# Kernel optimization log

Hardware: AMD Instinct MI355X
Metric: run time of the kernel (lower is better)

The kernel has to match this reference:

```python
import jax, jax.numpy as jnp
import numpy as np

B, S, D, H, HD = 2, 2048, 1024, 16, 64
DFF = 4 * D
EPS = 1e-6


def _rms(x, w):
    return w * (x * jax.lax.rsqrt(jnp.mean(x * x, axis=-1, keepdims=True) + EPS))


def _rope(x, rope):
    # x: [B, H, S, HD], rope: [S, HD, 2]
    cos = rope[..., 0][None, None]
    sin = rope[..., 1][None, None]
    xr = x.reshape(*x.shape[:-1], -1, 2)
    rot = jnp.stack([-xr[..., 1], xr[..., 0]], axis=-1).reshape(x.shape)
    return x * cos + rot * sin


def setup_inputs() -> dict:
    key = jax.random.key(0)
    ks = jax.random.split(key, 10)
    w = lambda k, shape: jax.random.normal(k, shape, jnp.float32) * 0.02
    return {
        "hidden_states": jax.random.normal(ks[0], (B, S, D), jnp.float32),
        "timestep": jax.random.normal(ks[1], (B, D), jnp.float32),
        "rope_pos_embed": jax.random.normal(ks[2], (S, HD, 2), jnp.float32),
        "adaln_w": w(ks[3], (6 * D, D)),
        "adaln_b": jnp.zeros((6 * D,), jnp.float32),
        "wq": w(ks[4], (D, D)),
        "wk": w(ks[5], (D, D)),
        "wv": w(ks[6], (D, D)),
        "wo": w(ks[7], (D, D)),
        "q_norm_w": jnp.ones((D,), jnp.float32),
        "k_norm_w": jnp.ones((D,), jnp.float32),
        "norm3_w": jnp.ones((D,), jnp.float32),
        "fc1_w": w(ks[8], (DFF, D)),
        "fc1_b": jnp.zeros((DFF,), jnp.float32),
        "fc2_w": w(ks[9], (D, DFF)),
        "fc2_b": jnp.zeros((D,), jnp.float32),
    }


def reference(hidden_states, timestep, rope_pos_embed, adaln_w, adaln_b,
              wq, wk, wv, wo, q_norm_w, k_norm_w, norm3_w,
              fc1_w, fc1_b, fc2_w, fc2_b):
    x = hidden_states  # [B, S, D]
    # AdaLayerNorm: emb = Linear(SiLU(timestep)) -> 6 modulation chunks, broadcast over seq
    emb = jax.nn.silu(timestep) @ adaln_w.T + adaln_b  # [B, 6D]
    sh_msa, sc_msa, g_msa, sh_mlp, sc_mlp, g_mlp = jnp.split(emb[:, None, :], 6, axis=-1)
    mu = jnp.mean(x, axis=-1, keepdims=True)
    var = jnp.mean((x - mu) ** 2, axis=-1, keepdims=True)
    ln = (x - mu) * jax.lax.rsqrt(var + EPS)
    xm = ln * (1.0 + sc_msa) + sh_msa  # modulated input to attention

    # Attention: projections + RMSNorm over inner_dim + RoPE + SDPA
    q = _rms(xm @ wq.T, q_norm_w)
    k = _rms(xm @ wk.T, k_norm_w)
    v = xm @ wv.T
    q = q.reshape(B, S, H, HD).transpose(0, 2, 1, 3)
    k = k.reshape(B, S, H, HD).transpose(0, 2, 1, 3)
    v = v.reshape(B, S, H, HD).transpose(0, 2, 1, 3)
    q = _rope(q, rope_pos_embed)
    k = _rope(k, rope_pos_embed)
    scores = jnp.einsum('bhqd,bhkd->bhqk', q, k) * (HD ** -0.5)
    attn = jax.nn.softmax(scores, axis=-1)
    o = jnp.einsum('bhqk,bhkd->bhqd', attn, v)
    o = o.transpose(0, 2, 1, 3).reshape(B, S, H * HD) @ wo.T

    h = x + g_msa * o  # gated residual

    # MLP branch with AdaLN scale/shift on RMSNorm output
    n3 = _rms(h, norm3_w)
    nm = n3 * (1.0 + sc_mlp) + sh_mlp
    ff = jax.nn.gelu(nm @ fc1_w.T + fc1_b, approximate=True) @ fc2_w.T + fc2_b
    return h + g_mlp * ff
```

## Files before the change

### kernel.cpp

```cpp
#include <hip/hip_runtime.h>
#include <cstdint>
#include <cstddef>

typedef unsigned short ushort_t;
typedef __attribute__((ext_vector_type(8))) short s8v;
typedef __attribute__((ext_vector_type(4))) short s4v;
typedef __attribute__((ext_vector_type(4))) float f4v;

#define MFMA16(a, b, c) __builtin_amdgcn_mfma_f32_16x16x32_bf16(a, b, c, 0, 0, 0)

__device__ __forceinline__ ushort_t f2bf(float f) {
  union { float f; unsigned u; } a; a.f = f;
  return (ushort_t)((a.u + 0x7fffu + ((a.u >> 16) & 1u)) >> 16);
}
__device__ __forceinline__ float bf2f(ushort_t h) {
  union { unsigned u; float f; } a; a.u = ((unsigned)h) << 16; return a.f;
}
__device__ __forceinline__ unsigned fbits(float f) {
  union { float f; unsigned u; } a; a.f = f; return a.u;
}

__device__ __forceinline__ void gload16(const void* g, void* l) {
  __builtin_amdgcn_global_load_lds(
      (__attribute__((address_space(1))) void*)(uintptr_t)g,
      (__attribute__((address_space(3))) void*)(unsigned)(uintptr_t)l,
      16, 0, 0);
}

__launch_bounds__(256)
__global__ void convert_w(const float* __restrict__ wq, const float* __restrict__ wk,
                          const float* __restrict__ wv, const float* __restrict__ wo,
                          const float* __restrict__ f1, const float* __restrict__ f2,
                          ushort_t* __restrict__ dqkv, ushort_t* __restrict__ dwo,
                          ushort_t* __restrict__ df1, ushort_t* __restrict__ df2)
{
  const int blk = blockIdx.x;
  const float* src; ushort_t* dst; int off;
  if      (blk < 1024) { src = wq; dst = dqkv;            off = blk; }
  else if (blk < 2048) { src = wk; dst = dqkv + 1048576;  off = blk - 1024; }
  else if (blk < 3072) { src = wv; dst = dqkv + 2097152;  off = blk - 2048; }
  else if (blk < 4096) { src = wo; dst = dwo;             off = blk - 3072; }
  else if (blk < 8192) { src = f1; dst = df1;             off = blk - 4096; }
  else                 { src = f2; dst = df2;             off = blk - 8192; }
  const int idx = off * 1024 + threadIdx.x * 4;
  float4 v = *(const float4*)(src + idx);
  s4v o;
  o[0] = (short)f2bf(v.x); o[1] = (short)f2bf(v.y);
  o[2] = (short)f2bf(v.z); o[3] = (short)f2bf(v.w);
  *(s4v*)(dst + idx) = o;
}

__launch_bounds__(256)
__global__ void adaln(const float* __restrict__ ts, const float* __restrict__ w,
                      const float* __restrict__ bias, float* __restrict__ emb)
{
  const int j = blockIdx.x * 4 + (threadIdx.x >> 6);
  const int lane = threadIdx.x & 63;
  const float* wr = w + (size_t)j * 1024;
  float s0 = 0.f, s1 = 0.f;
  for (int i = lane; i < 1024; i += 64) {
    const float wv = wr[i];
    const float t0 = ts[i], t1 = ts[1024 + i];
    const float e0 = __builtin_amdgcn_exp2f(-1.4426950409f * t0);
    const float e1 = __builtin_amdgcn_exp2f(-1.4426950409f * t1);
    s0 += wv * t0 * __builtin_amdgcn_rcpf(1.f + e0);
    s1 += wv * t1 * __builtin_amdgcn_rcpf(1.f + e1);
  }
  #pragma unroll
  for (int m = 32; m; m >>= 1) { s0 += __shfl_down(s0, m); s1 += __shfl_down(s1, m); }
  if (!lane) { emb[j] = s0 + bias[j]; emb[6144 + j] = s1 + bias[j]; }
}

__launch_bounds__(256)
__global__ void ln_mod(const float* __restrict__ x, const float* __restrict__ emb,
                       ushort_t* __restrict__ xm)
{
  const int row = blockIdx.x, b = row >> 11, tid = threadIdx.x;
  const float* xr = x + (size_t)row * 1024;
  const int c = tid * 4;
  float4 v = *(const float4*)(xr + c);
  float s  = v.x + v.y + v.z + v.w;
  float s2 = v.x*v.x + v.y*v.y + v.z*v.z + v.w*v.w;
  #pragma unroll
  for (int m = 32; m; m >>= 1) { s += __shfl_down(s, m); s2 += __shfl_down(s2, m); }
  __shared__ float red[8];
  const int wave = tid >> 6, lane = tid & 63;
  if (!lane) { red[wave] = s; red[4 + wave] = s2; }
  __syncthreads();
  const float mu = (red[0] + red[1] + red[2] + red[3]) * (1.f / 1024.f);
  const float ms = (red[4] + red[5] + red[6] + red[7]) * (1.f / 1024.f);
  const float rstd = rsqrtf(ms - mu * mu + 1e-6f);
  const float* sh = emb + b * 6144;
  const float* sc = emb + b * 6144 + 1024;
  float4 shv = *(const float4*)(sh + c);
  float4 scv = *(const float4*)(sc + c);
  s4v ov;
  ov[0] = (short)f2bf((v.x - mu) * rstd * (1.f + scv.x) + shv.x);
  ov[1] = (short)f2bf((v.y - mu) * rstd * (1.f + scv.y) + shv.y);
  ov[2] = (short)f2bf((v.z - mu) * rstd * (1.f + scv.z) + shv.z);
  ov[3] = (short)f2bf((v.w - mu) * rstd * (1.f + scv.w) + shv.w);
  *(s4v*)(xm + (size_t)row * 1024 + c) = ov;
}

template<int EPI, int TN>
__launch_bounds__(256, 4)
__global__ void gemm_bt(const ushort_t* __restrict__ A, const ushort_t* __restrict__ Bw,
                        int K, int N,
                        ushort_t* __restrict__ outb, float* __restrict__ outf,
                        const float* __restrict__ bias, const float* __restrict__ resid,
                        const float* __restrict__ emb, int gate_off)
{
  constexpr int JN = TN / 32;
  constexpr int BUFB = TN * 32;
  __shared__ ushort_t As0[128 * 32], As1[128 * 32];
  __shared__ ushort_t Bs0[BUFB],    Bs1[BUFB];
  const int tid = threadIdx.x;
  const int wave = tid >> 6, lane = tid & 63;
  const int quad = lane >> 4, r = lane & 15;
  const int m0 = blockIdx.y * 128, n0 = blockIdx.x * TN;
  const int wm = (wave >> 1) * 64, wn = (wave & 1) * (TN / 2);

  const int srow = wave * 16 + (lane >> 2);
  const int scol = (lane & 3) * 8;
  const ushort_t* ag = A  + (size_t)(m0 + srow) * K + scol;
  const ushort_t* bg = Bw + (size_t)(n0 + srow) * K + scol;
  const size_t rowK64 = (size_t)64 * K;

  f4v acc[4][JN] = {};

  auto stage = [&](ushort_t* as, ushort_t* bs) {
    gload16(ag,          as + wave * 512);
    gload16(ag + rowK64, as + wave * 512 + 2048);
    gload16(bg,          bs + wave * 512);
    if (TN == 128) gload16(bg + rowK64, bs + wave * 512 + 2048);
    ag += 32; bg += 32;
  };
  auto compute = [&](const ushort_t* ab, const ushort_t* bb) {
    s8v af[4], bf[JN];
    #pragma unroll
    for (int i = 0; i < 4; i++)
      af[i] = *(const s8v*)(ab + (wm + i * 16 + r) * 32 + quad * 8);
    #pragma unroll
    for (int j = 0; j < JN; j++)
      bf[j] = *(const s8v*)(bb + (wn + j * 16 + r) * 32 + quad * 8);
    #pragma unroll
    for (int i = 0; i < 4; i++)
      #pragma unroll
      for (int j = 0; j < JN; j++)
        acc[i][j] = MFMA16(af[i], bf[j], acc[i][j]);
  };

  stage(As0, Bs0);
  __syncthreads();
  const int R = (K >> 6) - 1;
  for (int it = 0; it < R; it++) {
    stage(As1, Bs1);
    compute(As0, Bs0);
    __syncthreads();
    stage(As0, Bs0);
    compute(As1, Bs1);
    __syncthreads();
  }
  stage(As1, Bs1);
  compute(As0, Bs0);
  __syncthreads();
  compute(As1, Bs1);

  const int bblk = m0 >> 11;
  float bj[JN], gj[JN];
  #pragma unroll
  for (int j = 0; j < JN; j++) {
    const int col = n0 + wn + j * 16 + r;
    bj[j] = (EPI == 2 || EPI == 3) ? bias[col] : 0.f;
    gj[j] = (EPI == 1 || EPI == 3) ? emb[bblk * 6144 + gate_off + col] : 0.f;
  }
  #pragma unroll
  for (int i = 0; i < 4; i++) {
    #pragma unroll
    for (int rr = 0; rr < 4; rr++) {
      const int row = m0 + wm + i * 16 + quad * 4 + rr;
      const size_t rbase = (size_t)row * N + n0 + wn;
      #pragma unroll
      for (int j = 0; j < JN; j++) {
        float v = acc[i][j][rr];
        const size_t idx = rbase + j * 16 + r;
        if (EPI == 0) {
          outb[idx] = f2bf(v);
        } else if (EPI == 1) {
          outf[idx] = resid[idx] + gj[j] * v;
        } else if (EPI == 2) {
          v += bj[j];
          const float t = fmaf(v * v, 0.1029436f, 2.3022083f);
          const float e = __builtin_amdgcn_exp2f(-v * t);
          outb[idx] = f2bf(v * __builtin_amdgcn_rcpf(1.f + e));
        } else {
          outf[idx] = resid[idx] + gj[j] * (v + bj[j]);
        }
      }
    }
  }
}

#define G8_PHASE(AB, BB, KS, MH, LOADB)                                       \
  {                                                                           \
    s8v af[4];                                                                \
    const int ck = ((((KS) << 2) | quad) ^ rx) << 3;                          \
    const ushort_t* Ap = (AB) + (wm + (MH) * 64 + r) * 64 + ck;               \
    af[0] = *(const s8v*)(Ap);                                                \
    af[1] = *(const s8v*)(Ap + 1024);                                         \
    af[2] = *(const s8v*)(Ap + 2048);                                         \
    af[3] = *(const s8v*)(Ap + 3072);                                         \
    if (LOADB) {                                                              \
      const ushort_t* Bp = (BB) + (wn + r) * 64 + ck;                         \
      bf[0] = *(const s8v*)(Bp);                                              \
      bf[1] = *(const s8v*)(Bp + 1024);                                       \
      bf[2] = *(const s8v*)(Bp + 2048);                                       \
      bf[3] = *(const s8v*)(Bp + 3072);                                       \
    }                                                                         \
    __builtin_amdgcn_s_barrier();                                             \
    __builtin_amdgcn_s_setprio(1);                                            \
    _Pragma("unroll")                                                         \
    for (int i_ = 0; i_ < 4; i_++) {                                          \
      _Pragma("unroll")                                                       \
      for (int j_ = 0; j_ < 4; j_++)                                          \
        acc[(MH) * 4 + i_][j_] = MFMA16(af[i_], bf[j_], acc[(MH) * 4 + i_][j_]); \
    }                                                                         \
    __builtin_amdgcn_s_setprio(0);                                            \
    __builtin_amdgcn_s_barrier();                                             \
  }

template<int EPI>
__launch_bounds__(512, 2)
__global__ void gemm8p(const ushort_t* __restrict__ A, const ushort_t* __restrict__ Bw,
                       int K, int N, ushort_t* __restrict__ outb,
                       const float* __restrict__ bias)
{
  __shared__ ushort_t Ash[2][256 * 64];
  __shared__ ushort_t Bsh[2][256 * 64];
  const int tid = threadIdx.x;
  const int wid = tid >> 6, lane = tid & 63;
  const int quad = lane >> 4, r = lane & 15, rx = r & 7;

  const int nwg = gridDim.x * gridDim.y;
  int wg = blockIdx.y * gridDim.x + blockIdx.x;
  wg = (wg & 7) * (nwg >> 3) + (wg >> 3);
  const int bx = wg % gridDim.x, by = wg / gridDim.x;
  const int m0 = by * 256, n0 = bx * 256;
  const int wm = (wid >> 2) * 128;
  const int wn = (wid & 3) * 64;

  const int srow = lane >> 3;
  const int scol = ((lane & 7) ^ srow) * 8;
  const ushort_t* ag = A  + (size_t)(m0 + wid * 32 + srow) * K + scol;
  const ushort_t* bg = Bw + (size_t)(n0 + wid * 32 + srow) * K + scol;
  const size_t row8K = (size_t)8 * K;

  f4v acc[8][4] = {};

  auto STAGE = [&](int buf, int kt) {
    const size_t ko = (size_t)kt * 64;
    ushort_t* Ad = &Ash[buf][wid * 2048];
    ushort_t* Bd = &Bsh[buf][wid * 2048];
    #pragma unroll
    for (int c = 0; c < 4; c++)
      gload16(ag + ko + c * row8K, Ad + c * 512);
    #pragma unroll
    for (int c = 0; c < 4; c++)
      gload16(bg + ko + c * row8K, Bd + c * 512);
  };

  STAGE(0, 0);
  STAGE(1, 1);
  asm volatile("s_waitcnt vmcnt(8)" ::: "memory");
  __builtin_amdgcn_s_barrier();

  const int NT = K >> 6;
  #pragma unroll 1
  for (int t = 0; t < NT; t += 2) {
    {
      const ushort_t* Ab = &Ash[0][0];
      const ushort_t* Bb = &Bsh[0][0];
      s8v bf[4];
      G8_PHASE(Ab, Bb, 0, 0, true);
      G8_PHASE(Ab, Bb, 0, 1, false);
      G8_PHASE(Ab, Bb, 1, 0, true);
      G8_PHASE(Ab, Bb, 1, 1, false);
      if (t + 2 < NT) {
        STAGE(0, t + 2);
        asm volatile("s_waitcnt vmcnt(8)" ::: "memory");
      } else {
        asm volatile("s_waitcnt vmcnt(0)" ::: "memory");
      }
      __builtin_amdgcn_s_barrier();
    }
    {
      const ushort_t* Ab = &Ash[1][0];
      const ushort_t* Bb = &Bsh[1][0];
      s8v bf[4];
      G8_PHASE(Ab, Bb, 0, 0, true);
      G8_PHASE(Ab, Bb, 0, 1, false);
      G8_PHASE(Ab, Bb, 1, 0, true);
      G8_PHASE(Ab, Bb, 1, 1, false);
      if (t + 3 < NT) {
        STAGE(1, t + 3);
        asm volatile("s_waitcnt vmcnt(8)" ::: "memory");
      } else {
        asm volatile("s_waitcnt vmcnt(0)" ::: "memory");
      }
      __builtin_amdgcn_s_barrier();
    }
  }

  float bj[4];
  #pragma unroll
  for (int j = 0; j < 4; j++)
    bj[j] = (EPI == 2) ? bias[n0 + wn + j * 16 + r] : 0.f;
  #pragma unroll
  for (int i = 0; i < 8; i++) {
    #pragma unroll
    for (int rr = 0; rr < 4; rr++) {
      const int row = m0 + wm + i * 16 + quad * 4 + rr;
      const size_t rbase = (size_t)row * N + n0 + wn;
      #pragma unroll
      for (int j = 0; j < 4; j++) {
        float v = acc[i][j][rr];
        const size_t idx = rbase + j * 16 + r;
        if (EPI == 0) {
          outb[idx] = f2bf(v);
        } else {
          v += bj[j];
          const float tt = fmaf(v * v, 0.1029436f, 2.3022083f);
          const float e = __builtin_amdgcn_exp2f(-v * tt);
          outb[idx] = f2bf(v * __builtin_amdgcn_rcpf(1.f + e));
        }
      }
    }
  }
}

__launch_bounds__(256)
__global__ void qkv_post(const ushort_t* __restrict__ qkv, const float* __restrict__ rope,
                         const float* __restrict__ qw, const float* __restrict__ kw,
                         ushort_t* __restrict__ q_r, ushort_t* __restrict__ k_r,
                         ushort_t* __restrict__ v_r)
{
  const int row = blockIdx.x, b = row >> 11, s = row & 2047, tid = threadIdx.x;
  const ushort_t* base = qkv + (size_t)row * 3072;
  const int c = tid * 4;
  s4v qv = *(const s4v*)(base + c);
  s4v kv = *(const s4v*)(base + 1024 + c);
  s4v vv = *(const s4v*)(base + 2048 + c);
  float qf[4], kf[4]; float sq = 0.f, sk = 0.f;
  #pragma unroll
  for (int i = 0; i < 4; i++) {
    qf[i] = bf2f((ushort_t)qv[i]); kf[i] = bf2f((ushort_t)kv[i]);
    sq += qf[i] * qf[i]; sk += kf[i] * kf[i];
  }
  #pragma unroll
  for (int m = 32; m; m >>= 1) { sq += __shfl_down(sq, m); sk += __shfl_down(sk, m); }
  __shared__ float red[8];
  const int wave = tid >> 6, lane = tid & 63;
  if (!lane) { red[wave] = sq; red[4 + wave] = sk; }
  __syncthreads();
  const float rq = rsqrtf((red[0]+red[1]+red[2]+red[3]) * (1.f/1024.f) + 1e-6f)
                   * 0.18033688011112042f;
  const float rk = rsqrtf((red[4]+red[5]+red[6]+red[7]) * (1.f/1024.f) + 1e-6f);

  const int h = c >> 6, d = c & 63;
  const float* rp = rope + ((size_t)s * 64 + d) * 2;
  float4 r01 = *(const float4*)(rp);
  float4 r23 = *(const float4*)(rp + 4);
  const float q0 = qf[0]*rq*qw[c], q1 = qf[1]*rq*qw[c+1];
  const float q2 = qf[2]*rq*qw[c+2], q3 = qf[3]*rq*qw[c+3];
  const float k0 = kf[0]*rk*kw[c], k1 = kf[1]*rk*kw[c+1];
  const float k2 = kf[2]*rk*kw[c+2], k3 = kf[3]*rk*kw[c+3];
  s4v qo, ko;
  qo[0] = (short)f2bf(q0 * r01.x - q1 * r01.y);
  qo[1] = (short)f2bf(q1 * r01.z + q0 * r01.w);
  qo[2] = (short)f2bf(q2 * r23.x - q3 * r23.y);
  qo[3] = (short)f2bf(q3 * r23.z + q2 * r23.w);
  ko[0] = (short)f2bf(k0 * r01.x - k1 * r01.y);
  ko[1] = (short)f2bf(k1 * r01.z + k0 * r01.w);
  ko[2] = (short)f2bf(k2 * r23.x - k3 * r23.y);
  ko[3] = (short)f2bf(k3 * r23.z + k2 * r23.w);
  const size_t rowbase = ((size_t)(b * 16 + h) * 2048 + s) * 64;
  const int d_s = (((d >> 3) ^ (s & 7)) << 3) | (d & 7);
  *(s4v*)(q_r + rowbase + d) = qo;
  *(s4v*)(k_r + rowbase + d_s) = ko;
  *(s4v*)(v_r + rowbase + d) = vv;
}

__launch_bounds__(256)
__global__ void vtrans(const ushort_t* __restrict__ v_r, ushort_t* __restrict__ v_t)
{
  const int bh = blockIdx.x >> 5, st = blockIdx.x & 31;
  const int s0 = st * 64;
  __shared__ ushort_t tile[64 * 72];
  const int tid = threadIdx.x;
  #pragma unroll
  for (int rep = 0; rep < 2; rep++) {
    const int idx = rep * 256 + tid;
    const int sr = idx >> 3, dc = (idx & 7) << 3;
    s8v val = *(const s8v*)(v_r + ((size_t)bh * 2048 + s0 + sr) * 64 + dc);
    *(s8v*)(tile + sr * 72 + dc) = val;
  }
  __syncthreads();
  #pragma unroll
  for (int rep = 0; rep < 2; rep++) {
    const int idx = rep * 256 + tid;
    const int d = idx >> 3;
    const int scs = (((idx & 7) ^ (d & 7)) << 3);
    s8v val;
    const int sc = (idx & 7) << 3;
    #pragma unroll
    for (int j = 0; j < 8; j++) val[j] = (short)tile[(sc + j) * 72 + d];
    *(s8v*)(v_t + ((size_t)bh * 64 + d) * 2048 + s0 + scs) = val;
  }
}

__launch_bounds__(256, 4)
__global__ void flash(const ushort_t* __restrict__ q_r, const ushort_t* __restrict__ k_r,
                      const ushort_t* __restrict__ v_t, ushort_t* __restrict__ attn)
{
  __shared__ ushort_t Ksh[2][64 * 64];
  __shared__ ushort_t Vsh[2][64 * 64];
  __shared__ ushort_t Psh[4][16 * 64];
  const int bh = blockIdx.x >> 5, qb = blockIdx.x & 31;
  const int tid = threadIdx.x, wave = tid >> 6, lane = tid & 63;
  const int quad = lane >> 4, r = lane & 15;
  const int rx = r & 7;
  const int q0 = qb * 64 + wave * 16;
  const size_t bhS = (size_t)bh * 2048;

  s8v aq0 = *(const s8v*)(q_r + (bhS + q0 + r) * 64 + quad * 8);
  s8v aq1 = *(const s8v*)(q_r + (bhS + q0 + r) * 64 + 32 + quad * 8);

  f4v o[4] = {};
  float mi = -1e30f, li = 0.f;

  const ushort_t* kg = k_r + (bhS + wave * 16 + (lane >> 3)) * 64 + (lane & 7) * 8;
  const ushort_t* vg = v_t + ((size_t)bh * 64 + wave * 16 + (lane >> 3)) * 2048
                       + (lane & 7) * 8;
  const int klo = wave * 1024 + lane * 8;
  const int vlo = wave * 1024 + lane * 8;
  ushort_t* pw = &Psh[wave][0];

  auto stage = [&](ushort_t* kbuf, ushort_t* vbuf, int kb) {
    #pragma unroll
    for (int c = 0; c < 2; c++) {
      gload16(kg + (size_t)(kb + c * 8) * 64, kbuf + klo + c * 512);
      gload16(vg + kb + (size_t)(c * 8) * 2048, vbuf + vlo + c * 512);
    }
  };

  auto step = [&](const ushort_t* Kc, const ushort_t* Vc) {
    f4v st[4];
    __builtin_amdgcn_s_setprio(1);
    #pragma unroll
    for (int t = 0; t < 4; t++) {
      const ushort_t* krow = Kc + (t * 16 + r) * 64;
      s8v k0 = *(const s8v*)(krow + ((quad ^ rx) << 3));
      s8v k1 = *(const s8v*)(krow + (((4 + quad) ^ rx) << 3));
      f4v z = {};
      z = MFMA16(k0, aq0, z);
      z = MFMA16(k1, aq1, z);
      st[t] = z;
    }
    __builtin_amdgcn_s_setprio(0);

    float m4[4];
    #pragma unroll
    for (int t = 0; t < 4; t++)
      m4[t] = fmaxf(fmaxf(st[t][0], st[t][1]), fmaxf(st[t][2], st[t][3]));
    float mloc = fmaxf(fmaxf(m4[0], m4[1]), fmaxf(m4[2], m4[3]));
    mloc = fmaxf(mloc, __shfl_xor(mloc, 16));
    mloc = fmaxf(mloc, __shfl_xor(mloc, 32));
    const float mn = fmaxf(mi, mloc);
    const float al = __builtin_amdgcn_exp2f(mi - mn);

    float p[4][4];
    uint2 pk[4];
    #pragma unroll
    for (int t = 0; t < 4; t++) {
      #pragma unroll
      for (int rr = 0; rr < 4; rr++)
        p[t][rr] = __builtin_amdgcn_exp2f(st[t][rr] - mn);
      const unsigned u0 = fbits(p[t][0]) + 0x8000u;
      const unsigned u1 = fbits(p[t][1]) + 0x8000u;
      const unsigned u2 = fbits(p[t][2]) + 0x8000u;
      const unsigned u3 = fbits(p[t][3]) + 0x8000u;
      pk[t].x = __builtin_amdgcn_perm(u1, u0, 0x07060302u);
      pk[t].y = __builtin_amdgcn_perm(u3, u2, 0x07060302u);
    }

    #pragma unroll
    for (int t = 0; t < 4; t++) {
      const int cw = t * 2 + (quad >> 1);
      const int sc = cw ^ rx;
      *(uint2*)(pw + r * 64 + (sc << 3) + (quad & 1) * 4) = pk[t];
    }

    float alo[4];
    #pragma unroll
    for (int rr = 0; rr < 4; rr++) alo[rr] = __shfl(al, quad * 4 + rr);
    #pragma unroll
    for (int nt = 0; nt < 4; nt++)
      #pragma unroll
      for (int rr = 0; rr < 4; rr++) o[nt][rr] *= alo[rr];

    float s4r[4];
    #pragma unroll
    for (int t = 0; t < 4; t++)
      s4r[t] = (p[t][0] + p[t][1]) + (p[t][2] + p[t][3]);
    float ls = (s4r[0] + s4r[1]) + (s4r[2] + s4r[3]);
    ls += __shfl_xor(ls, 16);
    ls += __shfl_xor(ls, 32);
    li = al * li + ls;
    mi = mn;

    asm volatile("s_waitcnt lgkmcnt(0)" ::: "memory");

    __builtin_amdgcn_s_setprio(1);
    #pragma unroll
    for (int kc = 0; kc < 2; kc++) {
      const int c = kc * 4 + quad;
      const int sc = c ^ rx;
      s8v ap = *(const s8v*)(pw + r * 64 + (sc << 3));
      #pragma unroll
      for (int nt = 0; nt < 4; nt++) {
        s8v bv = *(const s8v*)(Vc + (nt * 16 + r) * 64 + (sc << 3));
        o[nt] = MFMA16(ap, bv, o[nt]);
      }
    }
    __builtin_amdgcn_s_setprio(0);
  };

  stage(Ksh[0], Vsh[0], 0);
  __syncthreads();

  #pragma unroll 1
  for (int kb = 0; kb < 2048; kb += 128) {
    stage(Ksh[1], Vsh[1], kb + 64);
    step(Ksh[0], Vsh[0]);
    __syncthreads();
    if (kb + 128 < 2048) stage(Ksh[0], Vsh[0], kb + 128);
    step(Ksh[1], Vsh[1]);
    __syncthreads();
  }

  const int h = bh & 15, b = bh >> 4;
  const float linv = 1.f / li;
  #pragma unroll
  for (int rr = 0; rr < 4; rr++) {
    const float inv = __shfl(linv, quad * 4 + rr);
    const size_t orow = ((size_t)(b * 2048 + q0 + quad * 4 + rr)) * 1024 + h * 64;
    #pragma unroll
    for (int nt = 0; nt < 4; nt++)
      attn[orow + nt * 16 + r] = f2bf(o[nt][rr] * inv);
  }
}

__launch_bounds__(256)
__global__ void rms3_mod(const float* __restrict__ h, const float* __restrict__ emb,
                         const float* __restrict__ w3, ushort_t* __restrict__ nm)
{
  const int row = blockIdx.x, b = row >> 11, tid = threadIdx.x;
  const float* hr = h + (size_t)row * 1024;
  const int c = tid * 4;
  float4 v = *(const float4*)(hr + c);
  float s2 = v.x*v.x + v.y*v.y + v.z*v.z + v.w*v.w;
  #pragma unroll
  for (int m = 32; m; m >>= 1) s2 += __shfl_down(s2, m);
  __shared__ float red[4];
  const int wave = tid >> 6, lane = tid & 63;
  if (!lane) red[wave] = s2;
  __syncthreads();
  const float rms = rsqrtf((red[0] + red[1] + red[2] + red[3]) * (1.f / 1024.f) + 1e-6f);
  const float* sh = emb + b * 6144 + 3072;
  const float* sc = emb + b * 6144 + 4096;
  float4 shv = *(const float4*)(sh + c);
  float4 scv = *(const float4*)(sc + c);
  float4 wv  = *(const float4*)(w3 + c);
  s4v ov;
  ov[0] = (short)f2bf(v.x * rms * wv.x * (1.f + scv.x) + shv.x);
  ov[1] = (short)f2bf(v.y * rms * wv.y * (1.f + scv.y) + shv.y);
  ov[2] = (short)f2bf(v.z * rms * wv.z * (1.f + scv.z) + shv.z);
  ov[3] = (short)f2bf(v.w * rms * wv.w * (1.f + scv.w) + shv.w);
  *(s4v*)(nm + (size_t)row * 1024 + c) = ov;
}

extern "C" void kernel_launch(void* const* d_in, const int* in_sizes, int n_in,
                              void* d_out, int out_size, void* d_ws, size_t ws_size,
                              hipStream_t stream)
{
  const float* x    = (const float*)d_in[0];
  const float* ts   = (const float*)d_in[1];
  const float* rope = (const float*)d_in[2];
  const float* adw  = (const float*)d_in[3];
  const float* adb  = (const float*)d_in[4];
  const float* wq   = (const float*)d_in[5];
  const float* wk   = (const float*)d_in[6];
  const float* wv   = (const float*)d_in[7];
  const float* wo   = (const float*)d_in[8];
  const float* qnw  = (const float*)d_in[9];
  const float* knw  = (const float*)d_in[10];
  const float* n3w  = (const float*)d_in[11];
  const float* f1w  = (const float*)d_in[12];
  const float* f1b  = (const float*)d_in[13];
  const float* f2w  = (const float*)d_in[14];
  const float* f2b  = (const float*)d_in[15];

  char* ws = (char*)d_ws;
  ushort_t* WQKV = (ushort_t*)(ws + 0);
  ushort_t* WO   = (ushort_t*)(ws + 6291456);
  ushort_t* F1   = (ushort_t*)(ws + 8388608);
  ushort_t* F2   = (ushort_t*)(ws + 16777216);
  float*    EMB  = (float*)   (ws + 25165824);
  float*    H    = (float*)   (ws + 25214976);
  ushort_t* XM   = (ushort_t*)(ws + 41992192);
  ushort_t* QKV  = (ushort_t*)(ws + 50380800);
  ushort_t* QR   = (ushort_t*)(ws + 75546624);
  ushort_t* KR   = (ushort_t*)(ws + 83935232);
  ushort_t* VR   = (ushort_t*)(ws + 92323840);
  ushort_t* VT   = (ushort_t*)(ws + 100712448);
  ushort_t* ATTN = XM;
  ushort_t* NM   = QKV;
  ushort_t* FF1  = QR;

  convert_w<<<12288, 256, 0, stream>>>(wq, wk, wv, wo, f1w, f2w, WQKV, WO, F1, F2);
  adaln<<<1536, 256, 0, stream>>>(ts, adw, adb, EMB);
  ln_mod<<<4096, 256, 0, stream>>>(x, EMB, XM);
  gemm8p<0><<<dim3(12, 16), 512, 0, stream>>>(XM, WQKV, 1024, 3072, QKV, nullptr);
  qkv_post<<<4096, 256, 0, stream>>>(QKV, rope, qnw, knw, QR, KR, VR);
  vtrans<<<1024, 256, 0, stream>>>(VR, VT);
  flash<<<1024, 256, 0, stream>>>(QR, KR, VT, ATTN);
  gemm_bt<1, 64><<<dim3(16, 32), 256, 0, stream>>>(ATTN, WO, 1024, 1024,
      nullptr, H, nullptr, x, EMB, 2048);
  rms3_mod<<<4096, 256, 0, stream>>>(H, EMB, n3w, NM);
  gemm8p<2><<<dim3(16, 16), 512, 0, stream>>>(NM, F1, 1024, 4096, FF1, f1b);
  gemm_bt<3, 64><<<dim3(16, 32), 256, 0, stream>>>(FF1, F2, 4096, 1024,
      nullptr, (float*)d_out, f2b, H, EMB, 5120);
}
```

Before: 408.3 us.

## Load V fragments directly from global and skip softmax rescale when max is stable

The flash kernel no longer stages V tiles in shared memory. Each wave loads its V MFMA operands straight from global memory into registers at the start of each step, which removes the V LDS buffers and their reads. The online softmax also gains a lazy rescale: the running max and the accumulator rescale are updated only when some lane's new block max exceeds the old one by more than 8, so most steps skip the exp and multiplies. The GEMM phase macro adds an explicit LDS wait after the barrier. Direct global V loads add latency to every step and lean on cache hits, and the lazy rescale lets exponentials reach up to 2^8, which has a small accuracy risk.

```diff
diff --git a/kernel.cpp b/kernel.cpp
--- a/kernel.cpp
+++ b/kernel.cpp
@@ -218,6 +218,7 @@
       bf[3] = *(const s8v*)(Bp + 3072);                                       \
     }                                                                         \
     __builtin_amdgcn_s_barrier();                                             \
+    asm volatile("s_waitcnt lgkmcnt(0)" ::: "memory");                        \
     __builtin_amdgcn_s_setprio(1);                                            \
     _Pragma("unroll")                                                         \
     for (int i_ = 0; i_ < 4; i_++) {                                          \
@@ -423,7 +424,6 @@
                       const ushort_t* __restrict__ v_t, ushort_t* __restrict__ attn)
 {
   __shared__ ushort_t Ksh[2][64 * 64];
-  __shared__ ushort_t Vsh[2][64 * 64];
   __shared__ ushort_t Psh[4][16 * 64];
   const int bh = blockIdx.x >> 5, qb = blockIdx.x & 31;
   const int tid = threadIdx.x, wave = tid >> 6, lane = tid & 63;
@@ -439,21 +439,25 @@
   float mi = -1e30f, li = 0.f;
 
   const ushort_t* kg = k_r + (bhS + wave * 16 + (lane >> 3)) * 64 + (lane & 7) * 8;
-  const ushort_t* vg = v_t + ((size_t)bh * 64 + wave * 16 + (lane >> 3)) * 2048
-                       + (lane & 7) * 8;
   const int klo = wave * 1024 + lane * 8;
-  const int vlo = wave * 1024 + lane * 8;
+  const ushort_t* vb = v_t + ((size_t)bh * 64 + r) * 2048;
   ushort_t* pw = &Psh[wave][0];
 
-  auto stage = [&](ushort_t* kbuf, ushort_t* vbuf, int kb) {
-    #pragma unroll
-    for (int c = 0; c < 2; c++) {
-      gload16(kg + (size_t)(kb + c * 8) * 64, kbuf + klo + c * 512);
-      gload16(vg + kb + (size_t)(c * 8) * 2048, vbuf + vlo + c * 512);
-    }
+  auto stageK = [&](ushort_t* kbuf, int kb) {
+    gload16(kg + (size_t)kb * 64, kbuf + klo);
+    gload16(kg + (size_t)(kb + 8) * 64, kbuf + klo + 512);
   };
 
-  auto step = [&](const ushort_t* Kc, const ushort_t* Vc) {
+  auto step = [&](const ushort_t* Kc, ushort_t* Knext, int kb, int kbn) {
+    s8v bv0[4], bv1[4];
+    #pragma unroll
+    for (int nt = 0; nt < 4; nt++) {
+      const ushort_t* vrow = vb + (size_t)(nt * 16) * 2048 + kb;
+      bv0[nt] = *(const s8v*)(vrow + (((quad) ^ rx) << 3));
+      bv1[nt] = *(const s8v*)(vrow + (((4 + quad) ^ rx) << 3));
+    }
+    if (kbn >= 0) stageK(Knext, kbn);
+
     f4v st[4];
     __builtin_amdgcn_s_setprio(1);
     #pragma unroll
@@ -475,8 +479,9 @@
     float mloc = fmaxf(fmaxf(m4[0], m4[1]), fmaxf(m4[2], m4[3]));
     mloc = fmaxf(mloc, __shfl_xor(mloc, 16));
     mloc = fmaxf(mloc, __shfl_xor(mloc, 32));
-    const float mn = fmaxf(mi, mloc);
-    const float al = __builtin_amdgcn_exp2f(mi - mn);
+
+    const bool grow = !__all(mloc - mi <= 8.f);
+    const float mref = grow ? fmaxf(mi, mloc) : mi;
 
     float p[4][4];
     uint2 pk[4];
@@ -484,7 +489,7 @@
     for (int t = 0; t < 4; t++) {
       #pragma unroll
       for (int rr = 0; rr < 4; rr++)
-        p[t][rr] = __builtin_amdgcn_exp2f(st[t][rr] - mn);
+        p[t][rr] = __builtin_amdgcn_exp2f(st[t][rr] - mref);
       const unsigned u0 = fbits(p[t][0]) + 0x8000u;
       const unsigned u1 = fbits(p[t][1]) + 0x8000u;
       const unsigned u2 = fbits(p[t][2]) + 0x8000u;
@@ -500,13 +505,18 @@
       *(uint2*)(pw + r * 64 + (sc << 3) + (quad & 1) * 4) = pk[t];
     }
 
-    float alo[4];
-    #pragma unroll
-    for (int rr = 0; rr < 4; rr++) alo[rr] = __shfl(al, quad * 4 + rr);
-    #pragma unroll
-    for (int nt = 0; nt < 4; nt++)
+    if (grow) {
+      const float al = __builtin_amdgcn_exp2f(mi - mref);
+      float alo[4];
       #pragma unroll
-      for (int rr = 0; rr < 4; rr++) o[nt][rr] *= alo[rr];
+      for (int rr = 0; rr < 4; rr++) alo[rr] = __shfl(al, quad * 4 + rr);
+      #pragma unroll
+      for (int nt = 0; nt < 4; nt++)
+        #pragma unroll
+        for (int rr = 0; rr < 4; rr++) o[nt][rr] *= alo[rr];
+      li *= al;
+      mi = mref;
+    }
 
     float s4r[4];
     #pragma unroll
@@ -515,8 +525,7 @@
     float ls = (s4r[0] + s4r[1]) + (s4r[2] + s4r[3]);
     ls += __shfl_xor(ls, 16);
     ls += __shfl_xor(ls, 32);
-    li = al * li + ls;
-    mi = mn;
+    li += ls;
 
     asm volatile("s_waitcnt lgkmcnt(0)" ::: "memory");
 
@@ -527,24 +536,20 @@
       const int sc = c ^ rx;
       s8v ap = *(const s8v*)(pw + r * 64 + (sc << 3));
       #pragma unroll
-      for (int nt = 0; nt < 4; nt++) {
-        s8v bv = *(const s8v*)(Vc + (nt * 16 + r) * 64 + (sc << 3));
-        o[nt] = MFMA16(ap, bv, o[nt]);
-      }
+      for (int nt = 0; nt < 4; nt++)
+        o[nt] = MFMA16(ap, (kc == 0) ? bv0[nt] : bv1[nt], o[nt]);
     }
     __builtin_amdgcn_s_setprio(0);
   };
 
-  stage(Ksh[0], Vsh[0], 0);
+  stageK(Ksh[0], 0);
   __syncthreads();
 
   #pragma unroll 1
   for (int kb = 0; kb < 2048; kb += 128) {
-    stage(Ksh[1], Vsh[1], kb + 64);
-    step(Ksh[0], Vsh[0]);
+    step(Ksh[0], Ksh[1], kb, kb + 64);
     __syncthreads();
-    if (kb + 128 < 2048) stage(Ksh[0], Vsh[0], kb + 128);
-    step(Ksh[1], Vsh[1]);
+    step(Ksh[1], Ksh[0], kb + 64, (kb + 128 < 2048) ? kb + 128 : -1);
     __syncthreads();
   }
 
```

After: 426.3 us. 1.04x slower.
